# Optimization experiments

Hardware: AMD Instinct MI355X
Metric: run time of the kernel (lower is better)

The kernel has to match this reference:

```python
import jax, jax.numpy as jnp
import numpy as np

N = 100000
E = 600000
D = 128          # in_channels
D_OUT = 128      # out_channels


def setup_inputs() -> dict:
    key = jax.random.key(0)
    ks = jax.random.split(key, 8)
    node_embeddings = jax.random.normal(ks[0], (N, D), dtype=jnp.float32)
    edge_index = jax.random.randint(ks[1], (2, E), 0, N, dtype=jnp.int64)
    s = 1.0 / np.sqrt(D)
    W_src = jax.random.uniform(ks[2], (D, D), minval=-s, maxval=s, dtype=jnp.float32)
    W_tgt = jax.random.uniform(ks[3], (D, D), minval=-s, maxval=s, dtype=jnp.float32)
    s2 = 1.0 / np.sqrt(2 * D)
    W_proj = jax.random.uniform(ks[4], (2 * D, D_OUT), minval=-s2, maxval=s2, dtype=jnp.float32)
    b_proj = jax.random.uniform(ks[5], (D_OUT,), minval=-s2, maxval=s2, dtype=jnp.float32)
    s3 = 1.0 / np.sqrt(D_OUT)
    W_mlp = jax.random.uniform(ks[6], (D_OUT, D_OUT), minval=-s3, maxval=s3, dtype=jnp.float32)
    b_mlp = jax.random.uniform(ks[7], (D_OUT,), minval=-s3, maxval=s3, dtype=jnp.float32)
    return {
        "node_embeddings": node_embeddings,
        "edge_index": edge_index,
        "W_src": W_src,
        "W_tgt": W_tgt,
        "W_proj": W_proj,
        "b_proj": b_proj,
        "W_mlp": W_mlp,
        "b_mlp": b_mlp,
    }


def reference(node_embeddings, edge_index, W_src, W_tgt, W_proj, b_proj, W_mlp, b_mlp):
    src = node_embeddings[edge_index[0]]   # [E, D]
    tgt = node_embeddings[edge_index[1]]   # [E, D]
    gate_s = jax.nn.sigmoid(src @ W_src)   # Linear no bias + sigmoid
    gate_t = jax.nn.sigmoid(tgt @ W_tgt)
    attn_s = gate_s * src
    attn_t = gate_t * tgt
    edge_attr = jnp.concatenate([attn_s, attn_t], axis=-1)  # [E, 2D]
    edge_attr = edge_attr @ W_proj + b_proj                  # [E, D_OUT]
    return jax.nn.relu(edge_attr) @ W_mlp + b_mlp
```

## Files before the change

### kernel.cpp

```cpp
#include <hip/hip_runtime.h>

#define NN 100000
#define NE 600000
#define DD 128

typedef _Float16 half4_t __attribute__((ext_vector_type(4)));
typedef _Float16 half8_t __attribute__((ext_vector_type(8)));
typedef float f32x4 __attribute__((ext_vector_type(4)));

__device__ __forceinline__ int swzb(int row, int byte) {
  return row * 256 + (byte ^ ((row & 7) << 4));
}

__device__ __forceinline__ half8_t relu_add(half8_t a, half8_t b) {
  half8_t r;
#pragma unroll
  for (int j = 0; j < 8; ++j) {
    const _Float16 s = a[j] + b[j];
    r[j] = s > (_Float16)0 ? s : (_Float16)0;
  }
  return r;
}

__global__ void prep_kernel(const float* __restrict__ Wsrc,
                            const float* __restrict__ Wtgt,
                            const float* __restrict__ Wproj,
                            const float* __restrict__ Wmlp,
                            const unsigned int* __restrict__ eraw,
                            int* __restrict__ idx,
                            _Float16* __restrict__ packed) {
  const int bid = (int)blockIdx.x;
  const int tid = (int)threadIdx.x;
  if (bid < 40) {
    const int t = bid * 256 + tid;
    if (t >= 5 * 2048) return;
    const int m = t >> 11;
    const int rem = t & 2047;
    const int nf = rem >> 8;
    const int ks = (rem >> 6) & 3;
    const int l = rem & 63;
    const float* W;
    if (m == 0) W = Wsrc;
    else if (m == 1) W = Wtgt;
    else if (m == 2) W = Wproj;
    else if (m == 3) W = Wproj + 128 * DD;
    else W = Wmlp;
    const int col = (l & 15) + 16 * nf;
    const int k0 = 8 * (l >> 4) + 32 * ks;
    half8_t v;
#pragma unroll
    for (int j = 0; j < 8; ++j)
      v[j] = (_Float16)W[(size_t)(k0 + j) * DD + col];
    *reinterpret_cast<half8_t*>(packed + (size_t)m * 16384 +
                                (size_t)rem * 8) = v;
  } else {
    __shared__ int s_is64;
    if (tid < 64) {
      const unsigned long long b = __ballot(eraw[2 * tid + 1] != 0u);
      if (tid == 0) s_is64 = (b == 0ull) ? 1 : 0;
    }
    __syncthreads();
    const int is64 = s_is64;
    const size_t stride = (size_t)512 * 256;
    for (size_t i = (size_t)(bid - 40) * 256 + tid; i < 2 * (size_t)NE;
         i += stride)
      idx[i] = (int)(is64 ? eraw[2 * i] : eraw[i]);
  }
}

__global__ __launch_bounds__(256, 4)
void phase1_kernel(const float* __restrict__ Xg,
                   const _Float16* __restrict__ packW,
                   const float* __restrict__ bproj,
                   _Float16* __restrict__ Aout,
                   _Float16* __restrict__ Bout) {
  __shared__ _Float16 Xh[64 * DD];
  __shared__ _Float16 Th[64 * DD];
  const int tid = (int)threadIdx.x;
  const int row0 = (int)blockIdx.x * 64;
  const int rem = NN - row0;
  const int nvalid = rem < 64 ? rem : 64;

#pragma unroll
  for (int it = 0; it < 8; ++it) {
    const int i = tid + it * 256;
    const int r = i >> 5;
    const int c4 = i & 31;
    float4 v = make_float4(0.f, 0.f, 0.f, 0.f);
    if (r < nvalid)
      v = reinterpret_cast<const float4*>(Xg + (size_t)(row0 + r) * DD)[c4];
    half4_t h;
    h[0] = (_Float16)v.x; h[1] = (_Float16)v.y;
    h[2] = (_Float16)v.z; h[3] = (_Float16)v.w;
    *reinterpret_cast<half4_t*>(&Xh[swzb(r, c4 * 8) >> 1]) = h;
  }
  __syncthreads();

  const int l = tid & 63;
  const int w = tid >> 6;
  const int lr = l & 15;
  const int lg = l >> 4;

#pragma unroll 1
  for (int p = 0; p < 2; ++p) {
    const _Float16* __restrict__ wb1 = packW + (size_t)p * 16384 + l * 8;
    half8_t w1[2][4];
#pragma unroll
    for (int s = 0; s < 2; ++s)
#pragma unroll
      for (int ks = 0; ks < 4; ++ks)
        w1[s][ks] = *reinterpret_cast<const half8_t*>(
            wb1 + (size_t)(((2 * w + s) * 4 + ks)) * 512);

    f32x4 acc[4][2];
#pragma unroll
    for (int mf = 0; mf < 4; ++mf)
#pragma unroll
      for (int s = 0; s < 2; ++s) acc[mf][s] = (f32x4)0.f;
#pragma unroll
    for (int mf = 0; mf < 4; ++mf) {
      half8_t xf[4];
#pragma unroll
      for (int ks = 0; ks < 4; ++ks)
        xf[ks] = *reinterpret_cast<const half8_t*>(
            &Xh[swzb(mf * 16 + lr, lg * 16 + ks * 64) >> 1]);
#pragma unroll
      for (int ks = 0; ks < 4; ++ks)
#pragma unroll
        for (int s = 0; s < 2; ++s)
          acc[mf][s] = __builtin_amdgcn_mfma_f32_16x16x32_f16(
              w1[s][ks], xf[ks], acc[mf][s], 0, 0, 0);
    }

    if (p) __syncthreads();

#pragma unroll
    for (int mf = 0; mf < 4; ++mf)
#pragma unroll
      for (int s = 0; s < 2; ++s) {
        const int c0 = (2 * w + s) * 16 + lg * 4;
        const int node = mf * 16 + lr;
        const half4_t xh =
            *reinterpret_cast<const half4_t*>(&Xh[swzb(node, c0 * 2) >> 1]);
        half4_t th;
#pragma unroll
        for (int j = 0; j < 4; ++j) {
          const float t = (float)xh[j] / (1.f + __expf(-acc[mf][s][j]));
          th[j] = (_Float16)t;
        }
        *reinterpret_cast<half4_t*>(&Th[swzb(node, c0 * 2) >> 1]) = th;
      }
    __syncthreads();

    const _Float16* __restrict__ wb2 = packW + (size_t)(2 + p) * 16384 + l * 8;
    half8_t w2[2][4];
#pragma unroll
    for (int s = 0; s < 2; ++s)
#pragma unroll
      for (int ks = 0; ks < 4; ++ks)
        w2[s][ks] = *reinterpret_cast<const half8_t*>(
            wb2 + (size_t)(((2 * w + s) * 4 + ks)) * 512);

    f32x4 acc2[4][2];
#pragma unroll
    for (int mf = 0; mf < 4; ++mf)
#pragma unroll
      for (int s = 0; s < 2; ++s) acc2[mf][s] = (f32x4)0.f;
#pragma unroll
    for (int mf = 0; mf < 4; ++mf) {
      half8_t tf[4];
#pragma unroll
      for (int ks = 0; ks < 4; ++ks)
        tf[ks] = *reinterpret_cast<const half8_t*>(
            &Th[swzb(mf * 16 + lr, lg * 16 + ks * 64) >> 1]);
#pragma unroll
      for (int ks = 0; ks < 4; ++ks)
#pragma unroll
        for (int s = 0; s < 2; ++s)
          acc2[mf][s] = __builtin_amdgcn_mfma_f32_16x16x32_f16(
              w2[s][ks], tf[ks], acc2[mf][s], 0, 0, 0);
    }

    _Float16* __restrict__ dst = p ? Bout : Aout;
#pragma unroll
    for (int s = 0; s < 2; ++s) {
      const int c0 = (2 * w + s) * 16 + lg * 4;
      f32x4 bp = (f32x4)0.f;
      if (p == 0) bp = *reinterpret_cast<const f32x4*>(bproj + c0);
#pragma unroll
      for (int mf = 0; mf < 4; ++mf) {
        const int node = mf * 16 + lr;
        if (node < nvalid) {
          const f32x4 v = acc2[mf][s] + bp;
          half4_t h;
#pragma unroll
          for (int j = 0; j < 4; ++j) h[j] = (_Float16)v[j];
          *reinterpret_cast<half4_t*>(dst + (size_t)(row0 + node) * DD + c0) =
              h;
        }
      }
    }
  }
}

__global__ __launch_bounds__(256, 5)
void phase2_kernel(const _Float16* __restrict__ At,
                   const _Float16* __restrict__ Bt,
                   const int* __restrict__ idx,
                   const _Float16* __restrict__ Wpk,
                   const float* __restrict__ bmlp,
                   float* __restrict__ out) {
  __shared__ _Float16 Wl[16384];
  const int tid = (int)threadIdx.x;
  const int l = tid & 63;
  const int w = tid >> 6;
  const int lr = l & 15;
  const int lg = l >> 4;
  const int e0 = (int)blockIdx.x * 64;
  const int er = e0 + w * 16 + lr;

  const int ia = idx[er];
  const int ib = idx[(size_t)NE + er];
  const _Float16* __restrict__ pa = At + (size_t)ia * DD + lg * 8;
  const _Float16* __restrict__ pb = Bt + (size_t)ib * DD + lg * 8;
  half8_t af[4], bf[4];
#pragma unroll
  for (int ks = 0; ks < 4; ++ks) {
    af[ks] = *reinterpret_cast<const half8_t*>(pa + ks * 32);
    bf[ks] = *reinterpret_cast<const half8_t*>(pb + ks * 32);
  }

#pragma unroll
  for (int i = 0; i < 8; ++i) {
    const int c = tid + i * 256;
    reinterpret_cast<f32x4*>(Wl)[c] = reinterpret_cast<const f32x4*>(Wpk)[c];
  }

  f32x4 acc[8];
#pragma unroll
  for (int nf = 0; nf < 8; ++nf) acc[nf] = (f32x4)0.f;

  __syncthreads();

#pragma unroll
  for (int ks = 0; ks < 4; ++ks) {
    const half8_t r = relu_add(af[ks], bf[ks]);
#pragma unroll
    for (int nf = 0; nf < 8; ++nf) {
      const half8_t wf = *reinterpret_cast<const half8_t*>(
          &Wl[(size_t)(nf * 4 + ks) * 512 + l * 8]);
      acc[nf] =
          __builtin_amdgcn_mfma_f32_16x16x32_f16(wf, r, acc[nf], 0, 0, 0);
    }
  }

#pragma unroll
  for (int nf = 0; nf < 8; ++nf) {
    const int c0 = nf * 16 + lg * 4;
    acc[nf] = acc[nf] + *reinterpret_cast<const f32x4*>(bmlp + c0);
  }

  __syncthreads();

  float* __restrict__ tile = reinterpret_cast<float*>(Wl) + w * 2048;
#pragma unroll
  for (int nf = 0; nf < 8; ++nf) {
    const int o = nf * 64 + lg * 16;
    *reinterpret_cast<f32x4*>(
        reinterpret_cast<char*>(tile) + lr * 512 + (o ^ ((lr & 7) << 4))) =
        acc[nf];
  }
  float* __restrict__ gbase = out + (size_t)(e0 + w * 16) * DD;
#pragma unroll
  for (int i = 0; i < 8; ++i) {
    const int o = i * 1024 + l * 16;
    const int row = o >> 9;
    const int bi = o & 511;
    const f32x4 v = *reinterpret_cast<const f32x4*>(
        reinterpret_cast<const char*>(tile) + row * 512 +
        (bi ^ ((row & 7) << 4)));
    __builtin_nontemporal_store(
        v, reinterpret_cast<f32x4*>(reinterpret_cast<char*>(gbase) + o));
  }
}

extern "C" void kernel_launch(void* const* d_in, const int* in_sizes, int n_in,
                              void* d_out, int out_size, void* d_ws,
                              size_t ws_size, hipStream_t stream) {
  (void)in_sizes; (void)n_in; (void)out_size; (void)ws_size;

  const float* X = (const float*)d_in[0];
  const unsigned int* eraw = (const unsigned int*)d_in[1];
  const float* Wsrc = (const float*)d_in[2];
  const float* Wtgt = (const float*)d_in[3];
  const float* Wproj = (const float*)d_in[4];
  const float* bproj = (const float*)d_in[5];
  const float* Wmlp = (const float*)d_in[6];
  const float* bmlp = (const float*)d_in[7];
  float* out = (float*)d_out;

  _Float16* A16 = (_Float16*)d_ws;
  _Float16* B16 = A16 + (size_t)NN * DD;
  _Float16* packW = B16 + (size_t)NN * DD;
  int* idx = (int*)(packW + 5 * 16384);

  prep_kernel<<<552, 256, 0, stream>>>(Wsrc, Wtgt, Wproj, Wmlp, eraw, idx,
                                       packW);
  phase1_kernel<<<(NN + 63) / 64, 256, 0, stream>>>(X, packW, bproj, A16, B16);
  phase2_kernel<<<NE / 64, 256, 0, stream>>>(A16, B16, idx,
                                             packW + 4 * 16384, bmlp, out);
}
```

Before: 144.1 us.

## Move edge index conversion into phase1 and stage outputs via LDS for coalesced stores

The edge-index int64-to-int32 conversion moves out of the prep kernel into extra blocks of the phase1 launch, so it can overlap with the node projection work and the prep kernel shrinks to the weight packing only. Phase1 results are now written to shared memory first and then copied to global memory as full 16-byte nontemporal stores per row, replacing the scattered 8-byte stores. This costs extra barriers and an LDS round trip per pass.

```diff
diff --git a/kernel.cpp b/kernel.cpp
--- a/kernel.cpp
+++ b/kernel.cpp
@@ -3,6 +3,8 @@
 #define NN 100000
 #define NE 600000
 #define DD 128
+#define NB1 1563
+#define NDEC 512
 
 typedef _Float16 half4_t __attribute__((ext_vector_type(4)));
 typedef _Float16 half8_t __attribute__((ext_vector_type(8)));
@@ -26,58 +28,57 @@
                             const float* __restrict__ Wtgt,
                             const float* __restrict__ Wproj,
                             const float* __restrict__ Wmlp,
-                            const unsigned int* __restrict__ eraw,
-                            int* __restrict__ idx,
                             _Float16* __restrict__ packed) {
-  const int bid = (int)blockIdx.x;
-  const int tid = (int)threadIdx.x;
-  if (bid < 40) {
-    const int t = bid * 256 + tid;
-    if (t >= 5 * 2048) return;
-    const int m = t >> 11;
-    const int rem = t & 2047;
-    const int nf = rem >> 8;
-    const int ks = (rem >> 6) & 3;
-    const int l = rem & 63;
-    const float* W;
-    if (m == 0) W = Wsrc;
-    else if (m == 1) W = Wtgt;
-    else if (m == 2) W = Wproj;
-    else if (m == 3) W = Wproj + 128 * DD;
-    else W = Wmlp;
-    const int col = (l & 15) + 16 * nf;
-    const int k0 = 8 * (l >> 4) + 32 * ks;
-    half8_t v;
-#pragma unroll
-    for (int j = 0; j < 8; ++j)
-      v[j] = (_Float16)W[(size_t)(k0 + j) * DD + col];
-    *reinterpret_cast<half8_t*>(packed + (size_t)m * 16384 +
-                                (size_t)rem * 8) = v;
-  } else {
-    __shared__ int s_is64;
-    if (tid < 64) {
-      const unsigned long long b = __ballot(eraw[2 * tid + 1] != 0u);
-      if (tid == 0) s_is64 = (b == 0ull) ? 1 : 0;
-    }
-    __syncthreads();
-    const int is64 = s_is64;
-    const size_t stride = (size_t)512 * 256;
-    for (size_t i = (size_t)(bid - 40) * 256 + tid; i < 2 * (size_t)NE;
-         i += stride)
-      idx[i] = (int)(is64 ? eraw[2 * i] : eraw[i]);
-  }
+  const int t = (int)blockIdx.x * 256 + (int)threadIdx.x;
+  if (t >= 5 * 2048) return;
+  const int m = t >> 11;
+  const int rem = t & 2047;
+  const int nf = rem >> 8;
+  const int ks = (rem >> 6) & 3;
+  const int l = rem & 63;
+  const float* W;
+  if (m == 0) W = Wsrc;
+  else if (m == 1) W = Wtgt;
+  else if (m == 2) W = Wproj;
+  else if (m == 3) W = Wproj + 128 * DD;
+  else W = Wmlp;
+  const int col = (l & 15) + 16 * nf;
+  const int k0 = 8 * (l >> 4) + 32 * ks;
+  half8_t v;
+#pragma unroll
+  for (int j = 0; j < 8; ++j) v[j] = (_Float16)W[(size_t)(k0 + j) * DD + col];
+  *reinterpret_cast<half8_t*>(packed + (size_t)m * 16384 + (size_t)rem * 8) = v;
 }
 
 __global__ __launch_bounds__(256, 4)
 void phase1_kernel(const float* __restrict__ Xg,
                    const _Float16* __restrict__ packW,
                    const float* __restrict__ bproj,
+                   const unsigned int* __restrict__ eraw,
+                   int* __restrict__ idx,
                    _Float16* __restrict__ Aout,
                    _Float16* __restrict__ Bout) {
   __shared__ _Float16 Xh[64 * DD];
   __shared__ _Float16 Th[64 * DD];
+  __shared__ int s_is64;
   const int tid = (int)threadIdx.x;
-  const int row0 = (int)blockIdx.x * 64;
+  const int bid = (int)blockIdx.x;
+
+  if (bid >= NB1) {
+    if (tid < 64) {
+      const unsigned long long b = __ballot(eraw[2 * tid + 1] != 0u);
+      if (tid == 0) s_is64 = (b == 0ull) ? 1 : 0;
+    }
+    __syncthreads();
+    const int is64 = s_is64;
+    const size_t stride = (size_t)NDEC * 256;
+    for (size_t i = (size_t)(bid - NB1) * 256 + tid; i < 2 * (size_t)NE;
+         i += stride)
+      idx[i] = (int)(is64 ? eraw[2 * i] : eraw[i]);
+    return;
+  }
+
+  const int row0 = bid * 64;
   const int rem = NN - row0;
   const int nvalid = rem < 64 ? rem : 64;
 
@@ -132,8 +133,6 @@
               w1[s][ks], xf[ks], acc[mf][s], 0, 0, 0);
     }
 
-    if (p) __syncthreads();
-
 #pragma unroll
     for (int mf = 0; mf < 4; ++mf)
 #pragma unroll
@@ -181,7 +180,8 @@
               w2[s][ks], tf[ks], acc2[mf][s], 0, 0, 0);
     }
 
-    _Float16* __restrict__ dst = p ? Bout : Aout;
+    __syncthreads();
+
 #pragma unroll
     for (int s = 0; s < 2; ++s) {
       const int c0 = (2 * w + s) * 16 + lg * 4;
@@ -190,16 +190,30 @@
 #pragma unroll
       for (int mf = 0; mf < 4; ++mf) {
         const int node = mf * 16 + lr;
-        if (node < nvalid) {
-          const f32x4 v = acc2[mf][s] + bp;
-          half4_t h;
-#pragma unroll
-          for (int j = 0; j < 4; ++j) h[j] = (_Float16)v[j];
-          *reinterpret_cast<half4_t*>(dst + (size_t)(row0 + node) * DD + c0) =
-              h;
-        }
+        const f32x4 v = acc2[mf][s] + bp;
+        half4_t h;
+#pragma unroll
+        for (int j = 0; j < 4; ++j) h[j] = (_Float16)v[j];
+        *reinterpret_cast<half4_t*>(&Th[swzb(node, c0 * 2) >> 1]) = h;
       }
     }
+    __syncthreads();
+
+    _Float16* __restrict__ dst = p ? Bout : Aout;
+    char* __restrict__ gb =
+        reinterpret_cast<char*>(dst) + (size_t)row0 * 256;
+#pragma unroll
+    for (int it = 0; it < 4; ++it) {
+      const int o = it * 4096 + tid * 16;
+      if (o < nvalid * 256) {
+        const int rowi = o >> 8;
+        const int col = o & 255;
+        const f32x4 v = *reinterpret_cast<const f32x4*>(
+            reinterpret_cast<const char*>(Th) + swzb(rowi, col));
+        __builtin_nontemporal_store(v, reinterpret_cast<f32x4*>(gb + o));
+      }
+    }
+    __syncthreads();
   }
 }
 
@@ -304,9 +318,9 @@
   _Float16* packW = B16 + (size_t)NN * DD;
   int* idx = (int*)(packW + 5 * 16384);
 
-  prep_kernel<<<552, 256, 0, stream>>>(Wsrc, Wtgt, Wproj, Wmlp, eraw, idx,
-                                       packW);
-  phase1_kernel<<<(NN + 63) / 64, 256, 0, stream>>>(X, packW, bproj, A16, B16);
+  prep_kernel<<<40, 256, 0, stream>>>(Wsrc, Wtgt, Wproj, Wmlp, packW);
+  phase1_kernel<<<NB1 + NDEC, 256, 0, stream>>>(X, packW, bproj, eraw, idx,
+                                                A16, B16);
   phase2_kernel<<<NE / 64, 256, 0, stream>>>(A16, B16, idx,
                                              packW + 4 * 16384, bmlp, out);
 }
```

Result: slower. 150.6 us (+4.5%).
